# Kernel optimization log

Measured on AMD Instinct MI355X. Metric: run time of the kernel, lower is better.

Reference implementation:

```python
import jax, jax.numpy as jnp
import numpy as np

EMB_DIM = 128
WEIGHT_COL = 24

def setup_inputs() -> dict:
    key = jax.random.key(0)
    ks = jax.random.split(key, 9)
    B, S = 8, 4096
    s_in = 1.0 / np.sqrt(EMB_DIM)
    s_out = 1.0 / np.sqrt(WEIGHT_COL)
    return {
        "x": jax.random.normal(ks[0], (B, S, EMB_DIM), dtype=jnp.float32),
        "wQ": jax.random.uniform(ks[1], (EMB_DIM, WEIGHT_COL), jnp.float32, -s_in, s_in),
        "bQ": jax.random.uniform(ks[2], (WEIGHT_COL,), jnp.float32, -s_in, s_in),
        "wK": jax.random.uniform(ks[3], (EMB_DIM, WEIGHT_COL), jnp.float32, -s_in, s_in),
        "bK": jax.random.uniform(ks[4], (WEIGHT_COL,), jnp.float32, -s_in, s_in),
        "wV": jax.random.uniform(ks[5], (EMB_DIM, WEIGHT_COL), jnp.float32, -s_in, s_in),
        "bV": jax.random.uniform(ks[6], (WEIGHT_COL,), jnp.float32, -s_in, s_in),
        "wO": jax.random.uniform(ks[7], (WEIGHT_COL, EMB_DIM), jnp.float32, -s_out, s_out),
        "bO": jax.random.uniform(ks[8], (EMB_DIM,), jnp.float32, -s_out, s_out),
    }

def reference(x, wQ, bQ, wK, bK, wV, bV, wO, bO):
    # projections: [B,S,E] -> [B,S,D]
    Q = x @ wQ + bQ
    K = x @ wK + bK
    V = x @ wV + bV
    # NOTE: source scales by sqrt(emb_dim), not sqrt(weight_col)
    scale = 1.0 / np.sqrt(EMB_DIM).astype(np.float32)
    scores = jnp.einsum('bqd,bkd->bqk', Q, K) * scale  # [B,S,S]
    A = jax.nn.softmax(scores, axis=-1)
    H = jnp.einsum('bqk,bkd->bqd', A, V)               # [B,S,D]
    return H @ wO + bO                                  # [B,S,E]
```

## Files before the change

### kernel.cpp

```cpp
#include <hip/hip_runtime.h>
#include <hip/hip_fp16.h>


#define B_ 8
#define S_ 4096
#define E_ 128
#define D_ 24
#define N_ (B_ * S_)
#define SCALE 0.08838834764831845f
#define LOG2E 1.4426950408889634f

#define HS_STRIDE 40
#define XS_STRIDE 136
#define OS_STRIDE 84

typedef __attribute__((ext_vector_type(8))) short bfrag;
typedef __attribute__((ext_vector_type(4))) float ffrag;

__device__ inline unsigned short f2bf(float f) {
    unsigned int x = __builtin_bit_cast(unsigned int, f);
    return (unsigned short)((x + 0x7fffu + ((x >> 16) & 1u)) >> 16);
}
__device__ inline unsigned int pack2h(float a, float b) {
    unsigned int ua = __builtin_bit_cast(unsigned int, a) + 0x8000u;
    unsigned int ub = __builtin_bit_cast(unsigned int, b) + 0x8000u;
    return __builtin_amdgcn_perm(ub, ua, 0x07060302);
}
__device__ inline unsigned int packh16(float a, float b) {
    return __builtin_bit_cast(unsigned int, __builtin_amdgcn_cvt_pkrtz(a, b));
}

__global__ __launch_bounds__(256) void prep_kernel(
    const float* __restrict__ wQ, const float* __restrict__ bQ,
    const float* __restrict__ wK, const float* __restrict__ bK,
    const float* __restrict__ wV, const float* __restrict__ bV,
    const float* __restrict__ wO,
    unsigned short* __restrict__ Wf, unsigned short* __restrict__ wOf,
    float* __restrict__ bqkv)
{
    const int gtid   = blockIdx.x * 256 + threadIdx.x;
    const int stride = gridDim.x * 256;
    const float qs = SCALE * LOG2E;
    for (int idx = gtid; idx < 4 * 5 * 512; idx += stride) {
        const int j    = idx & 7;
        const int lane = (idx >> 3) & 63;
        const int nt   = (idx >> 9) % 5;
        const int kt   = idx / 2560;
        const int n = nt * 16 + (lane & 15);
        const int k = kt * 32 + ((lane >> 4) << 3) + j;
        float v = 0.0f;
        if (n < 24)      v = wQ[k * 24 + n] * qs;
        else if (n < 48) v = wK[k * 24 + (n - 24)];
        else if (n < 72) v = wV[k * 24 + (n - 48)];
        Wf[idx] = f2bf(v);
    }
    for (int idx = gtid; idx < 8 * 512; idx += stride) {
        const int j    = idx & 7;
        const int lane = (idx >> 3) & 63;
        const int nt   = idx >> 9;
        const int k = ((lane >> 4) << 3) + j;
        const int e = nt * 16 + (lane & 15);
        wOf[idx] = (k < 24) ? f2bf(wO[k * 128 + e]) : (unsigned short)0;
    }
    if (gtid < 80) {
        float v = 0.0f;
        if (gtid < 24)      v = bQ[gtid] * qs;
        else if (gtid < 48) v = bK[gtid - 24];
        else if (gtid < 72) v = bV[gtid - 48];
        bqkv[gtid] = v;
    }
}

__global__ __launch_bounds__(256) void proj_kernel(
    const float* __restrict__ x, const unsigned short* __restrict__ Wf,
    const float* __restrict__ bqkv,
    unsigned short* __restrict__ Qbf, unsigned short* __restrict__ Kbf,
    unsigned short* __restrict__ Vt)
{
    __shared__ float smem[64 * OS_STRIDE];
    unsigned short* xs = (unsigned short*)smem;
    float* os = smem;

    const int tid  = threadIdx.x;
    const int lane = tid & 63;
    const int w    = tid >> 6;
    const int col  = lane & 15;
    const int quad = lane >> 4;
    const int rb   = blockIdx.x * 64;

    #pragma unroll
    for (int i = 0; i < 8; ++i) {
        const int idx = i * 256 + tid;
        const int row = idx >> 5, c4 = idx & 31;
        const float4 xv = *(const float4*)(x + (size_t)(rb + row) * 128 + c4 * 4);
        uint2 h;
        h.x = pack2h(xv.x, xv.y);
        h.y = pack2h(xv.z, xv.w);
        *(uint2*)(&xs[row * XS_STRIDE + c4 * 4]) = h;
    }

    bfrag Wfr[20];
    #pragma unroll
    for (int f = 0; f < 20; ++f)
        Wfr[f] = *(const bfrag*)(Wf + (f * 64 + lane) * 8);

    __syncthreads();

    ffrag acc[5];
    #pragma unroll
    for (int nt = 0; nt < 5; ++nt) acc[nt] = (ffrag){0.f, 0.f, 0.f, 0.f};

    #pragma unroll
    for (int kt = 0; kt < 4; ++kt) {
        const bfrag Af = *(const bfrag*)(&xs[(w * 16 + col) * XS_STRIDE + kt * 32 + quad * 8]);
        #pragma unroll
        for (int nt = 0; nt < 5; ++nt)
            acc[nt] = __builtin_amdgcn_mfma_f32_16x16x32_bf16(Af, Wfr[kt * 5 + nt], acc[nt], 0, 0, 0);
    }

    __syncthreads();

    #pragma unroll
    for (int nt = 0; nt < 5; ++nt) {
        const float bb = bqkv[nt * 16 + col];
        #pragma unroll
        for (int r = 0; r < 4; ++r)
            os[(w * 16 + quad * 4 + r) * OS_STRIDE + nt * 16 + col] = acc[nt][r] + bb;
    }
    __syncthreads();

    {
        const int half  = tid & 1;
        const int row   = (tid >> 1) & 63;
        const int isK   = tid >> 7;
        const int cbase = isK * 24;
        unsigned int pk[8];
        #pragma unroll
        for (int g = 0; g < 8; ++g) {
            const int c0 = half * 16 + g * 2;
            const float f0 = (c0     < 24) ? os[row * OS_STRIDE + cbase + c0]     : 0.0f;
            const float f1 = (c0 + 1 < 24) ? os[row * OS_STRIDE + cbase + c0 + 1] : 0.0f;
            pk[g] = pack2h(f0, f1);
        }
        unsigned short* dst = (isK ? Kbf : Qbf) + (size_t)(rb + row) * 32 + half * 16;
        *(uint4*)(dst)     = make_uint4(pk[0], pk[1], pk[2], pk[3]);
        *(uint4*)(dst + 8) = make_uint4(pk[4], pk[5], pk[6], pk[7]);
    }

    if (tid < 192) {
        const int d  = tid % 24;
        const int ch = tid / 24;
        unsigned int p[4];
        #pragma unroll
        for (int g = 0; g < 4; ++g) {
            const float f0 = os[(ch * 8 + g * 2 + 0) * OS_STRIDE + 48 + d];
            const float f1 = os[(ch * 8 + g * 2 + 1) * OS_STRIDE + 48 + d];
            p[g] = pack2h(f0, f1);
        }
        const int b = rb >> 12, s0 = rb & 4095;
        uint4* dst = (uint4*)(Vt + (((size_t)(b * 32 + d)) << 12) + s0 + ch * 8);
        *dst = make_uint4(p[0], p[1], p[2], p[3]);
    } else if (tid < 200) {
        const int ch = tid - 192;
        const int b = rb >> 12, s0 = rb & 4095;
        uint4* dst = (uint4*)(Vt + (((size_t)(b * 32 + 24)) << 12) + s0 + ch * 8);
        *dst = make_uint4(0x3F803F80u, 0x3F803F80u, 0x3F803F80u, 0x3F803F80u);
    }
}

__global__ __launch_bounds__(256, 4) void attn_kernel(
    const unsigned short* __restrict__ Qbf, const unsigned short* __restrict__ Kbf,
    const unsigned short* __restrict__ Vt,
    __half* __restrict__ Opart, float* __restrict__ lpart)
{
    const int tid    = threadIdx.x;
    const int lane   = tid & 63;
    const int w      = tid >> 6;
    const int col    = lane & 15;
    const int quad   = lane >> 4;
    const int blk    = blockIdx.x;
    const int split  = blockIdx.y;
    const int kchunk = S_ / gridDim.y;
    const int b      = blk >> 5;
    const int qbase  = blk * 128 + w * 32;

    const bfrag Qf0 = *(const bfrag*)(Qbf + (size_t)(qbase + col) * 32 + quad * 8);
    const bfrag Qf1 = *(const bfrag*)(Qbf + (size_t)(qbase + 16 + col) * 32 + quad * 8);

    const int keyE = ((col >> 2) << 3) + (col & 3);
    const unsigned short* Kp =
        Kbf + ((size_t)b * 4096 + (size_t)split * kchunk + keyE) * 32 + quad * 8;
    const int d1 = (16 + col <= 24) ? (16 + col) : 24;
    const unsigned short* Vp0 =
        Vt + ((size_t)(b * 32 + col)) * 4096 + (size_t)split * kchunk + quad * 8;
    const unsigned short* Vp1 =
        Vt + ((size_t)(b * 32 + d1)) * 4096 + (size_t)split * kchunk + quad * 8;

    ffrag O00 = {0.f,0.f,0.f,0.f};
    ffrag O01 = {0.f,0.f,0.f,0.f};
    ffrag O10 = {0.f,0.f,0.f,0.f};
    ffrag O11 = {0.f,0.f,0.f,0.f};

    #pragma unroll 2
    for (int it = 0; it < kchunk; it += 32) {
        const bfrag Kfe = *(const bfrag*)(Kp);
        const bfrag Kfo = *(const bfrag*)(Kp + 128);
        const bfrag Va0 = *(const bfrag*)(Vp0);
        const bfrag Va1 = *(const bfrag*)(Vp1);
        Kp += 1024; Vp0 += 32; Vp1 += 32;

        {
            ffrag Se = {0.f,0.f,0.f,0.f}, So = {0.f,0.f,0.f,0.f};
            Se = __builtin_amdgcn_mfma_f32_16x16x32_bf16(Kfe, Qf0, Se, 0, 0, 0);
            So = __builtin_amdgcn_mfma_f32_16x16x32_bf16(Kfo, Qf0, So, 0, 0, 0);
            union { bfrag f; unsigned int u[4]; } P;
            P.u[0] = pack2h(__builtin_amdgcn_exp2f(Se[0]), __builtin_amdgcn_exp2f(Se[1]));
            P.u[1] = pack2h(__builtin_amdgcn_exp2f(Se[2]), __builtin_amdgcn_exp2f(Se[3]));
            P.u[2] = pack2h(__builtin_amdgcn_exp2f(So[0]), __builtin_amdgcn_exp2f(So[1]));
            P.u[3] = pack2h(__builtin_amdgcn_exp2f(So[2]), __builtin_amdgcn_exp2f(So[3]));
            O00 = __builtin_amdgcn_mfma_f32_16x16x32_bf16(Va0, P.f, O00, 0, 0, 0);
            O01 = __builtin_amdgcn_mfma_f32_16x16x32_bf16(Va1, P.f, O01, 0, 0, 0);
        }
        {
            ffrag Se = {0.f,0.f,0.f,0.f}, So = {0.f,0.f,0.f,0.f};
            Se = __builtin_amdgcn_mfma_f32_16x16x32_bf16(Kfe, Qf1, Se, 0, 0, 0);
            So = __builtin_amdgcn_mfma_f32_16x16x32_bf16(Kfo, Qf1, So, 0, 0, 0);
            union { bfrag f; unsigned int u[4]; } P;
            P.u[0] = pack2h(__builtin_amdgcn_exp2f(Se[0]), __builtin_amdgcn_exp2f(Se[1]));
            P.u[1] = pack2h(__builtin_amdgcn_exp2f(Se[2]), __builtin_amdgcn_exp2f(Se[3]));
            P.u[2] = pack2h(__builtin_amdgcn_exp2f(So[0]), __builtin_amdgcn_exp2f(So[1]));
            P.u[3] = pack2h(__builtin_amdgcn_exp2f(So[2]), __builtin_amdgcn_exp2f(So[3]));
            O10 = __builtin_amdgcn_mfma_f32_16x16x32_bf16(Va0, P.f, O10, 0, 0, 0);
            O11 = __builtin_amdgcn_mfma_f32_16x16x32_bf16(Va1, P.f, O11, 0, 0, 0);
        }
    }

    {
        const size_t base0 = ((size_t)split * N_ + qbase + col) * 32;
        uint2 s0;
        s0.x = packh16(O00[0], O00[1]);
        s0.y = packh16(O00[2], O00[3]);
        *(uint2*)(Opart + base0 + quad * 4) = s0;
        if (quad < 2) {
            uint2 s1;
            s1.x = packh16(O01[0], O01[1]);
            s1.y = packh16(O01[2], O01[3]);
            *(uint2*)(Opart + base0 + 16 + quad * 4) = s1;
        }
        if (quad == 2)
            lpart[(size_t)split * N_ + qbase + col] = O01[0];

        const size_t base1 = base0 + 16 * 32;
        uint2 t0;
        t0.x = packh16(O10[0], O10[1]);
        t0.y = packh16(O10[2], O10[3]);
        *(uint2*)(Opart + base1 + quad * 4) = t0;
        if (quad < 2) {
            uint2 t1;
            t1.x = packh16(O11[0], O11[1]);
            t1.y = packh16(O11[2], O11[3]);
            *(uint2*)(Opart + base1 + 16 + quad * 4) = t1;
        }
        if (quad == 2)
            lpart[(size_t)split * N_ + qbase + 16 + col] = O11[0];
    }
}

__global__ __launch_bounds__(256) void combine_kernel(
    const __half* __restrict__ Opart, const float* __restrict__ lpart,
    const unsigned short* __restrict__ wOf, const float* __restrict__ bO,
    float* __restrict__ out, int nsp)
{
    __shared__ unsigned short Hs[64 * HS_STRIDE];

    const int tid = threadIdx.x;
    const int qb  = blockIdx.x * 64;
    {
        const int ql = tid >> 2;
        const int c8 = (tid & 3) * 8;
        const int q  = qb + ql;
        float a[8] = {0.f, 0.f, 0.f, 0.f, 0.f, 0.f, 0.f, 0.f};
        if (c8 < 24) {
            for (int s = 0; s < nsp; ++s) {
                const __half2* p2 = (const __half2*)(Opart + ((size_t)s * N_ + q) * 32 + c8);
                #pragma unroll
                for (int j = 0; j < 4; ++j) {
                    const float2 f = __half22float2(p2[j]);
                    a[2 * j]     += f.x;
                    a[2 * j + 1] += f.y;
                }
            }
        }
        float ls = 0.f;
        for (int s = 0; s < nsp; ++s) ls += lpart[(size_t)s * N_ + q];
        const float inv = 1.0f / ls;
        uint4 pk;
        pk.x = pack2h(a[0] * inv, a[1] * inv);
        pk.y = pack2h(a[2] * inv, a[3] * inv);
        pk.z = pack2h(a[4] * inv, a[5] * inv);
        pk.w = pack2h(a[6] * inv, a[7] * inv);
        *(uint4*)(&Hs[ql * HS_STRIDE + c8]) = pk;
    }
    __syncthreads();

    const int lane = tid & 63;
    const int w    = tid >> 6;
    const int col  = lane & 15;
    const int quad = lane >> 4;
    const bfrag Hf = *(const bfrag*)(&Hs[(w * 16 + col) * HS_STRIDE + quad * 8]);
    #pragma unroll
    for (int nt = 0; nt < 8; ++nt) {
        const bfrag Wo = *(const bfrag*)(wOf + (nt * 64 + lane) * 8);
        ffrag C = {0.f, 0.f, 0.f, 0.f};
        C = __builtin_amdgcn_mfma_f32_16x16x32_bf16(Hf, Wo, C, 0, 0, 0);
        const float bo = bO[nt * 16 + col];
        #pragma unroll
        for (int r = 0; r < 4; ++r)
            out[(size_t)(qb + w * 16 + quad * 4 + r) * 128 + nt * 16 + col] = C[r] + bo;
    }
}

extern "C" void kernel_launch(void* const* d_in, const int* in_sizes, int n_in,
                              void* d_out, int out_size, void* d_ws, size_t ws_size,
                              hipStream_t stream) {
    const float* x  = (const float*)d_in[0];
    const float* wQ = (const float*)d_in[1];
    const float* bQ = (const float*)d_in[2];
    const float* wK = (const float*)d_in[3];
    const float* bK = (const float*)d_in[4];
    const float* wV = (const float*)d_in[5];
    const float* bV = (const float*)d_in[6];
    const float* wO = (const float*)d_in[7];
    const float* bO = (const float*)d_in[8];
    float* out = (float*)d_out;

    unsigned short* ws16 = (unsigned short*)d_ws;
    unsigned short* Qbf = ws16;
    unsigned short* Kbf = Qbf + (size_t)N_ * 32;
    unsigned short* Vt  = Kbf + (size_t)N_ * 32;
    unsigned short* Wf  = Vt + (size_t)B_ * 32 * S_;
    unsigned short* wOf = Wf + 4 * 5 * 512;
    float* bqkv = (float*)(wOf + 8 * 512);
    __half* Opart = (__half*)(bqkv + 80);
    const size_t baseBytes = (size_t)((char*)Opart - (char*)d_ws);

    int nsp = 4;
    while (nsp > 1) {
        const size_t need = baseBytes + (size_t)nsp * N_ * 32 * 2 + (size_t)nsp * N_ * 4;
        if (need <= ws_size) break;
        nsp >>= 1;
    }
    float* lpart = (float*)(Opart + (size_t)nsp * N_ * 32);

    prep_kernel<<<8, 256, 0, stream>>>(wQ, bQ, wK, bK, wV, bV, wO, Wf, wOf, bqkv);
    proj_kernel<<<N_ / 64, 256, 0, stream>>>(x, Wf, bqkv, Qbf, Kbf, Vt);
    attn_kernel<<<dim3(N_ / 128, nsp), 256, 0, stream>>>(Qbf, Kbf, Vt, Opart, lpart);
    combine_kernel<<<N_ / 64, 256, 0, stream>>>(Opart, lpart, wOf, bO, out, nsp);
}
```

Baseline: 138.0 us.

## Software-pipeline K/V fragment loads, raise occupancy hint and key splits

The attention loop now prefetches the next iteration's K and V fragments into registers before running the current MFMA/exp2 work, so global load latency can overlap with compute. Launch bounds are raised from 4 to 6 waves-per-EU blocks to push the compiler toward fewer registers and higher occupancy. The split-K count goes from 4 to 8, doubling grid parallelism at the cost of more partial outputs written and combined. The extra prefetch registers may conflict with the tighter register budget and could cause spills.

```diff
diff --git a/kernel.cpp b/kernel.cpp
--- a/kernel.cpp
+++ b/kernel.cpp
@@ -168,7 +168,7 @@
     }
 }
 
-__global__ __launch_bounds__(256, 4) void attn_kernel(
+__global__ __launch_bounds__(256, 6) void attn_kernel(
     const unsigned short* __restrict__ Qbf, const unsigned short* __restrict__ Kbf,
     const unsigned short* __restrict__ Vt,
     __half* __restrict__ Opart, float* __restrict__ lpart)
@@ -201,38 +201,49 @@
     ffrag O10 = {0.f,0.f,0.f,0.f};
     ffrag O11 = {0.f,0.f,0.f,0.f};
 
+    bfrag cKfe = *(const bfrag*)(Kp);
+    bfrag cKfo = *(const bfrag*)(Kp + 128);
+    bfrag cVa0 = *(const bfrag*)(Vp0);
+    bfrag cVa1 = *(const bfrag*)(Vp1);
+
     #pragma unroll 2
     for (int it = 0; it < kchunk; it += 32) {
-        const bfrag Kfe = *(const bfrag*)(Kp);
-        const bfrag Kfo = *(const bfrag*)(Kp + 128);
-        const bfrag Va0 = *(const bfrag*)(Vp0);
-        const bfrag Va1 = *(const bfrag*)(Vp1);
-        Kp += 1024; Vp0 += 32; Vp1 += 32;
+        bfrag nKfe, nKfo, nVa0, nVa1;
+        const bool more = (it + 32) < kchunk;
+        if (more) {
+            Kp += 1024; Vp0 += 32; Vp1 += 32;
+            nKfe = *(const bfrag*)(Kp);
+            nKfo = *(const bfrag*)(Kp + 128);
+            nVa0 = *(const bfrag*)(Vp0);
+            nVa1 = *(const bfrag*)(Vp1);
+        }
 
         {
             ffrag Se = {0.f,0.f,0.f,0.f}, So = {0.f,0.f,0.f,0.f};
-            Se = __builtin_amdgcn_mfma_f32_16x16x32_bf16(Kfe, Qf0, Se, 0, 0, 0);
-            So = __builtin_amdgcn_mfma_f32_16x16x32_bf16(Kfo, Qf0, So, 0, 0, 0);
+            Se = __builtin_amdgcn_mfma_f32_16x16x32_bf16(cKfe, Qf0, Se, 0, 0, 0);
+            So = __builtin_amdgcn_mfma_f32_16x16x32_bf16(cKfo, Qf0, So, 0, 0, 0);
             union { bfrag f; unsigned int u[4]; } P;
             P.u[0] = pack2h(__builtin_amdgcn_exp2f(Se[0]), __builtin_amdgcn_exp2f(Se[1]));
             P.u[1] = pack2h(__builtin_amdgcn_exp2f(Se[2]), __builtin_amdgcn_exp2f(Se[3]));
             P.u[2] = pack2h(__builtin_amdgcn_exp2f(So[0]), __builtin_amdgcn_exp2f(So[1]));
             P.u[3] = pack2h(__builtin_amdgcn_exp2f(So[2]), __builtin_amdgcn_exp2f(So[3]));
-            O00 = __builtin_amdgcn_mfma_f32_16x16x32_bf16(Va0, P.f, O00, 0, 0, 0);
-            O01 = __builtin_amdgcn_mfma_f32_16x16x32_bf16(Va1, P.f, O01, 0, 0, 0);
+            O00 = __builtin_amdgcn_mfma_f32_16x16x32_bf16(cVa0, P.f, O00, 0, 0, 0);
+            O01 = __builtin_amdgcn_mfma_f32_16x16x32_bf16(cVa1, P.f, O01, 0, 0, 0);
         }
         {
             ffrag Se = {0.f,0.f,0.f,0.f}, So = {0.f,0.f,0.f,0.f};
-            Se = __builtin_amdgcn_mfma_f32_16x16x32_bf16(Kfe, Qf1, Se, 0, 0, 0);
-            So = __builtin_amdgcn_mfma_f32_16x16x32_bf16(Kfo, Qf1, So, 0, 0, 0);
+            Se = __builtin_amdgcn_mfma_f32_16x16x32_bf16(cKfe, Qf1, Se, 0, 0, 0);
+            So = __builtin_amdgcn_mfma_f32_16x16x32_bf16(cKfo, Qf1, So, 0, 0, 0);
             union { bfrag f; unsigned int u[4]; } P;
             P.u[0] = pack2h(__builtin_amdgcn_exp2f(Se[0]), __builtin_amdgcn_exp2f(Se[1]));
             P.u[1] = pack2h(__builtin_amdgcn_exp2f(Se[2]), __builtin_amdgcn_exp2f(Se[3]));
             P.u[2] = pack2h(__builtin_amdgcn_exp2f(So[0]), __builtin_amdgcn_exp2f(So[1]));
             P.u[3] = pack2h(__builtin_amdgcn_exp2f(So[2]), __builtin_amdgcn_exp2f(So[3]));
-            O10 = __builtin_amdgcn_mfma_f32_16x16x32_bf16(Va0, P.f, O10, 0, 0, 0);
-            O11 = __builtin_amdgcn_mfma_f32_16x16x32_bf16(Va1, P.f, O11, 0, 0, 0);
-        }
+            O10 = __builtin_amdgcn_mfma_f32_16x16x32_bf16(cVa0, P.f, O10, 0, 0, 0);
+            O11 = __builtin_amdgcn_mfma_f32_16x16x32_bf16(cVa1, P.f, O11, 0, 0, 0);
+        }
+
+        cKfe = nKfe; cKfo = nKfo; cVa0 = nVa0; cVa1 = nVa1;
     }
 
     {
@@ -344,7 +355,7 @@
     __half* Opart = (__half*)(bqkv + 80);
     const size_t baseBytes = (size_t)((char*)Opart - (char*)d_ws);
 
-    int nsp = 4;
+    int nsp = 8;
     while (nsp > 1) {
         const size_t need = baseBytes + (size_t)nsp * N_ * 32 * 2 + (size_t)nsp * N_ * 4;
         if (need <= ws_size) break;
```

Measured after the change: 141.9 us. 2.8% more time.
